# Performance work log

Measured on AMD Instinct MI355X. Metric: run time of the kernel, lower is better.

## Reference

```python
import jax, jax.numpy as jnp
import numpy as np

C, S, K, SIGMA = 512, 11, 3, 16
B = 128
EPS = 1e-5  # BatchNorm eps (eval mode, running_mean=0, running_var=1)


def _make_dct_weight(Cc, H, W):
    # FcaNet 'low16' frequency selection
    lx = [0, 0, 1, 1, 0, 2, 2, 1, 2, 0, 3, 4, 0, 1, 3, 0]
    ly = [0, 1, 0, 1, 2, 0, 1, 2, 2, 3, 0, 0, 4, 3, 1, 5]
    mx = [u * (H // 7) for u in lx]
    my = [v * (W // 7) for v in ly]
    w = np.zeros((Cc, H, W), np.float32)
    cp = Cc // len(lx)

    def bf(pos, freq, POS):
        r = np.cos(np.pi * freq * (pos + 0.5) / POS) / np.sqrt(POS)
        return r if freq == 0 else r * np.sqrt(2.0)

    for i, (u, v) in enumerate(zip(mx, my)):
        for tx in range(H):
            for ty in range(W):
                w[i * cp:(i + 1) * cp, tx, ty] = bf(tx, u, H) * bf(ty, v, W)
    return jnp.asarray(w)


def _bn(f, g, b):
    # eval-mode BatchNorm2d: (f - 0)/sqrt(1+eps)*g + b, per channel (axis 1)
    s = g / jnp.sqrt(1.0 + EPS)
    return f * s[None, :, None, None] + b[None, :, None, None]


def _conv1x1(f, w, b):
    return jnp.einsum('bchw,oc->bohw', f, w) + b[None, :, None, None]


def _spatial_kernel(f, w_conv, b_conv, g_sp, b_sp):
    Bn = f.shape[0]
    s = _conv1x1(f, w_conv, b_conv)                  # (B, K*K, S, S)
    s = s.reshape(Bn, K * K, S * S).transpose(0, 2, 1)  # (B, S*S, K*K)
    s = _bn(s.reshape(Bn, S * S, K, K), g_sp, b_sp)
    return s.reshape(Bn, S * S, K * K)


def _channel_kernel(f, dct_w, fc1, fc2, g_ch, b_ch):
    y = jnp.sum(f * dct_w[None], axis=(-2, -1))      # (B, C) DCT pooling
    y = jax.nn.sigmoid(jax.nn.relu(y @ fc1.T) @ fc2.T)  # (B, C*K*K)
    y = _bn(y.reshape(-1, C, K, K), g_ch, b_ch)
    return y.reshape(-1, C, K * K)


def _unfold(f):
    # torch-style per-pixel kxk neighborhoods -> (B, C, H, W, K, K)
    p = (K + 1) // 2 - 1
    Bn, Cn, H, W = f.shape
    fp = jnp.pad(f, ((0, 0), (0, 0), (p, p), (p, p)))
    pat = jnp.stack([fp[:, :, di:di + H, dj:dj + W]
                     for di in range(K) for dj in range(K)], axis=-1)
    return pat.reshape(Bn, Cn, H, W, K, K)


def setup_inputs() -> dict:
    key = jax.random.key(0)
    ks = iter(jax.random.split(key, 32))

    def nrm(shape, s=0.02):
        return s * jax.random.normal(next(ks), shape, jnp.float32)

    def gma(shape):
        return 1.0 + 0.1 * jax.random.normal(next(ks), shape, jnp.float32)

    return dict(
        x=jax.random.normal(next(ks), (B, C, S, S), jnp.float32),
        dct_w=_make_dct_weight(C, S, S),
        w_conv=nrm((K * K, C)), b_conv=nrm((K * K,)),
        g_sp=gma((S * S,)), b_sp=nrm((S * S,), 0.05),
        g_ch=gma((C,)), b_ch=nrm((C,), 0.05),
        fc1=nrm((C // SIGMA, C)), fc2=nrm((C * K * K, C // SIGMA)),
        up_w1=nrm((2 * C, C)), up_b1=nrm((2 * C,)), up_g1=gma((2 * C,)), up_bb1=nrm((2 * C,), 0.05),
        up_w2=nrm((2 * C, 2 * C)), up_b2=nrm((2 * C,)), up_g2=gma((2 * C,)), up_bb2=nrm((2 * C,), 0.05),
        lo_w1=nrm((2 * C, 2 * C)), lo_b1=nrm((2 * C,)), lo_g1=gma((2 * C,)), lo_bb1=nrm((2 * C,), 0.05),
        lo_w2=nrm((C, 2 * C)), lo_b2=nrm((C,)), lo_g2=gma((C,)), lo_bb2=nrm((C,), 0.05),
    )


def reference(x, dct_w, w_conv, b_conv, g_sp, b_sp, g_ch, b_ch, fc1, fc2,
              up_w1, up_b1, up_g1, up_bb1, up_w2, up_b2, up_g2, up_bb2,
              lo_w1, lo_b1, lo_g1, lo_bb1, lo_w2, lo_b2, lo_g2, lo_bb2):
    Bn = x.shape[0]
    # instance kernel: spatial (B,1,HW,KK) x channel (B,C,1,KK)
    sk = _spatial_kernel(x, w_conv, b_conv, g_sp, b_sp)[:, None]
    ck = _channel_kernel(x, dct_w, fc1, fc2, g_ch, b_ch)[:, :, None]
    inst = (sk * ck).reshape(Bn, C, S, S, K, K)
    # CLM task representation (sum over batch between upper and lower)
    a = jax.nn.relu(_bn(_conv1x1(x, up_w1, up_b1), up_g1, up_bb1))
    a = jax.nn.relu(_bn(_conv1x1(a, up_w2, up_b2), up_g2, up_bb2))
    a = a.sum(axis=0, keepdims=True)
    a = jax.nn.relu(_bn(_conv1x1(a, lo_w1, lo_b1), lo_g1, lo_bb1))
    task_s = jax.nn.sigmoid(_bn(_conv1x1(a, lo_w2, lo_b2), lo_g2, lo_bb2))
    # task kernel (shared across the batch)
    sk_t = _spatial_kernel(task_s, w_conv, b_conv, g_sp, b_sp)[:, None]
    ck_t = _channel_kernel(task_s, dct_w, fc1, fc2, g_ch, b_ch)[:, :, None]
    task_kernel = (sk_t * ck_t).reshape(1, C, S, S, K, K)
    kernel = task_kernel * inst
    adapted = (_unfold(x) * kernel).mean(axis=(-1, -2))  # (B,C,S,S)
    return adapted + x, task_kernel
```

## Files before the change

### kernel.cpp

```cpp
#include <hip/hip_runtime.h>
#include <hip/hip_bf16.h>
#include <math.h>

#define BNEPS 1e-5f
#define BDIM_B 128
#define CDIM 512
#define SS 121
#define KK 9
#define MROWS (BDIM_B * SS)

typedef unsigned short u16;
typedef __bf16 bf16x8 __attribute__((ext_vector_type(8)));
typedef float f32x4 __attribute__((ext_vector_type(4)));

__device__ __forceinline__ u16 f2bf(float f) {
    union { float f; unsigned int u; } v; v.f = f;
    unsigned int r = v.u + 0x7FFF + ((v.u >> 16) & 1);
    return (u16)(r >> 16);
}
__device__ __forceinline__ float bf2f(u16 v) {
    union { unsigned int u; float f; } x; x.u = ((unsigned int)v) << 16; return x.f;
}

__device__ __forceinline__ void gld16(const u16* g, u16* l) {
    __builtin_amdgcn_global_load_lds(
        (const __attribute__((address_space(1))) void*)g,
        (__attribute__((address_space(3))) void*)l, 16, 0, 0);
}

template<int MODE, int SWIZ>
__global__ __launch_bounds__(256)
void gemm_mfma(const u16* __restrict__ A, const u16* __restrict__ Bw,
               const float* __restrict__ bias, const float* __restrict__ g,
               const float* __restrict__ bb, void* __restrict__ out,
               int Kd, int N, int NT)
{
    __shared__ __align__(16) u16 Als[2][128 * 32];
    __shared__ __align__(16) u16 Bls[2][128 * 32];

    const int tid  = threadIdx.x;
    const int lane = tid & 63;
    const int w    = tid >> 6;
    const int wm   = w >> 1, wn = w & 1;

    int bx, by;
    if (SWIZ) {
        int i = blockIdx.x;
        if (i < 960) {
            int xg = i & 7;
            int j  = i >> 3;
            bx = xg * 15 + (j >> 3);
            by = j & 7;
        } else { bx = 120; by = i - 960; }
    } else {
        bx = blockIdx.x / NT; by = blockIdx.x - bx * NT;
    }
    const int bm = bx * 128;
    const int bn = by * 128;

    f32x4 acc[4][4] = {};

    const int subrow = tid >> 2;
    const int kq     = tid & 3;
    const int gchunk = kq ^ ((subrow >> 1) & 3);
    const u16* Ab = A  + (size_t)(bm + subrow) * Kd + gchunk * 8;
    const u16* Bb = Bw + (size_t)(bn + subrow) * Kd + gchunk * 8;

    const int fa_row = wm * 64 + (lane & 15);
    const int fb_row = wn * 64 + (lane & 15);
    const int kofs   = (((lane >> 4) ^ (((lane & 15) >> 1) & 3))) * 8;

    const int NK = Kd >> 5;

#define STG(bf_, t_) do { \
    gld16(Ab + (size_t)(t_) * 32,                 &Als[bf_][(w * 16) * 32]); \
    gld16(Ab + (size_t)64 * Kd + (size_t)(t_) * 32, &Als[bf_][(w * 16 + 64) * 32]); \
    gld16(Bb + (size_t)(t_) * 32,                 &Bls[bf_][(w * 16) * 32]); \
    gld16(Bb + (size_t)64 * Kd + (size_t)(t_) * 32, &Bls[bf_][(w * 16 + 64) * 32]); \
} while (0)

    STG(0, 0);
    __syncthreads();
    int cur = 0;
    for (int t = 0; t < NK; ++t) {
        if (t + 1 < NK) STG(cur ^ 1, t + 1);
        bf16x8 af[4], bfv[4];
        #pragma unroll
        for (int i = 0; i < 4; ++i)
            af[i] = *(const bf16x8*)&Als[cur][(fa_row + i * 16) * 32 + kofs];
        #pragma unroll
        for (int j = 0; j < 4; ++j)
            bfv[j] = *(const bf16x8*)&Bls[cur][(fb_row + j * 16) * 32 + kofs];
        #pragma unroll
        for (int i = 0; i < 4; ++i)
            #pragma unroll
            for (int j = 0; j < 4; ++j)
                acc[i][j] = __builtin_amdgcn_mfma_f32_16x16x32_bf16(af[i], bfv[j], acc[i][j], 0, 0, 0);
        __syncthreads();
        cur ^= 1;
    }
#undef STG

    const float inv = 1.0f / sqrtf(1.0f + BNEPS);

    if (MODE == 1) {
        u16* Y = (u16*)out;
        int dstrow[4][4];
        #pragma unroll
        for (int i = 0; i < 4; ++i) {
            int mb = bm + wm * 64 + i * 16 + (lane >> 4) * 4;
            #pragma unroll
            for (int r = 0; r < 4; ++r) {
                int m = mb + r;
                int b = m / 121, p = m - b * 121;
                dstrow[i][r] = p * 128 + b;
            }
        }
        #pragma unroll
        for (int j = 0; j < 4; ++j) {
            int n = bn + wn * 64 + j * 16 + (lane & 15);
            float sc = g[n] * inv, bo = bias[n], bv = bb[n];
            #pragma unroll
            for (int i = 0; i < 4; ++i)
                #pragma unroll
                for (int r = 0; r < 4; ++r) {
                    float v = (acc[i][j][r] + bo) * sc + bv;
                    v = fmaxf(v, 0.0f);
                    Y[(size_t)dstrow[i][r] * N + n] = f2bf(v);
                }
        }
    } else {
        float ps[4];
        #pragma unroll
        for (int j = 0; j < 4; ++j) {
            int n = bn + wn * 64 + j * 16 + (lane & 15);
            float sc = g[n] * inv, bo = bias[n], bv = bb[n];
            float s = 0.f;
            #pragma unroll
            for (int i = 0; i < 4; ++i)
                #pragma unroll
                for (int r = 0; r < 4; ++r) {
                    float v = (acc[i][j][r] + bo) * sc + bv;
                    s += fmaxf(v, 0.0f);
                }
            ps[j] = s;
        }
        __syncthreads();
        float* red = (float*)Als;
        #pragma unroll
        for (int j = 0; j < 4; ++j)
            red[(wm * 4 + (lane >> 4)) * 128 + wn * 64 + j * 16 + (lane & 15)] = ps[j];
        __syncthreads();
        if (tid < 128) {
            float s = 0.f;
            #pragma unroll
            for (int r = 0; r < 8; ++r) s += red[r * 128 + tid];
            ((u16*)out)[(size_t)bx * N + bn + tid] = f2bf(s);
        }
    }
}

template<int MODE>
__device__ __forceinline__ void gemm_small_body(
    const u16* __restrict__ A, const u16* __restrict__ Bw,
    const float* __restrict__ bias, const float* __restrict__ g,
    const float* __restrict__ bb, u16* __restrict__ Y,
    int Kd, int N, int bn)
{
    const int tid  = threadIdx.x;
    const int lane = tid & 63;
    const int w    = tid >> 6;
    const int fr   = lane & 15;
    const int kq   = lane >> 4;
    const int r0   = w * 32;

    f32x4 acc[2][4] = {};
    const u16* a0p = A + (size_t)(r0 + fr) * Kd + kq * 8;
    const u16* a1p = a0p + (size_t)16 * Kd;
    const u16* bp  = Bw + (size_t)(bn + fr) * Kd + kq * 8;

    #pragma unroll 4
    for (int k0 = 0; k0 < Kd; k0 += 32) {
        bf16x8 a0 = *(const bf16x8*)(a0p + k0);
        bf16x8 a1 = *(const bf16x8*)(a1p + k0);
        #pragma unroll
        for (int j = 0; j < 4; ++j) {
            bf16x8 bv = *(const bf16x8*)(bp + (size_t)j * 16 * Kd + k0);
            acc[0][j] = __builtin_amdgcn_mfma_f32_16x16x32_bf16(a0, bv, acc[0][j], 0, 0, 0);
            acc[1][j] = __builtin_amdgcn_mfma_f32_16x16x32_bf16(a1, bv, acc[1][j], 0, 0, 0);
        }
    }

    const float inv = 1.0f / sqrtf(1.0f + BNEPS);
    #pragma unroll
    for (int j = 0; j < 4; ++j) {
        int n = bn + j * 16 + (lane & 15);
        float sc = g[n] * inv, bo = bias[n], bv = bb[n];
        #pragma unroll
        for (int t = 0; t < 2; ++t)
            #pragma unroll
            for (int r = 0; r < 4; ++r) {
                int m = r0 + t * 16 + (lane >> 4) * 4 + r;
                float v = (acc[t][j][r] + bo) * sc + bv;
                if (MODE == 3) v = fmaxf(v, 0.0f);
                else           v = 1.f / (1.f + expf(-v));
                Y[(size_t)m * N + n] = f2bf(v);
            }
    }
}

template<int MODE>
__global__ __launch_bounds__(256)
void gemm_small(const u16* __restrict__ A, const u16* __restrict__ Bw,
                const float* __restrict__ bias, const float* __restrict__ g,
                const float* __restrict__ bb, u16* __restrict__ Y,
                int Kd, int N)
{
    gemm_small_body<MODE>(A, Bw, bias, g, bb, Y, Kd, N, blockIdx.x * 64);
}

__device__ __forceinline__ void spatial_body(
    const u16* __restrict__ Arow, const u16* __restrict__ wcb,
    const float* __restrict__ b_conv, const float* __restrict__ g_sp,
    const float* __restrict__ b_sp, float* __restrict__ skb,
    bool task, int blk, float* __restrict__ skt)
{
    const float inv = 1.0f / sqrtf(1.0f + BNEPS);
    const int tid  = threadIdx.x;
    const int lane = tid & 63;
    const int w    = tid >> 6;
    const int fr   = lane & 15;
    const int kq   = lane >> 4;
    const int r0   = w * 32;

    f32x4 acc0 = {}, acc1 = {};
    const u16* a0p = Arow + (size_t)(r0 + fr) * 512 + kq * 8;
    const u16* a1p = a0p + (size_t)16 * 512;
    const u16* bp  = wcb + (size_t)fr * 512 + kq * 8;
    #pragma unroll
    for (int k0 = 0; k0 < 512; k0 += 32) {
        bf16x8 a0 = *(const bf16x8*)(a0p + k0);
        bf16x8 a1 = *(const bf16x8*)(a1p + k0);
        bf16x8 b  = *(const bf16x8*)(bp + k0);
        acc0 = __builtin_amdgcn_mfma_f32_16x16x32_bf16(a0, b, acc0, 0, 0, 0);
        acc1 = __builtin_amdgcn_mfma_f32_16x16x32_bf16(a1, b, acc1, 0, 0, 0);
    }

    int n = lane & 15;
    if (n < 9) {
        float bo = b_conv[n];
        #pragma unroll
        for (int t = 0; t < 2; ++t) {
            f32x4 a = t ? acc1 : acc0;
            #pragma unroll
            for (int r = 0; r < 4; ++r) {
                int mloc = r0 + t * 16 + (lane >> 4) * 4 + r;
                if (!task) {
                    int m = blk * 128 + mloc;
                    int p = m % 121;
                    float v = (a[r] + bo) * (g_sp[p] * inv) + b_sp[p];
                    skb[(size_t)m * 9 + n] = v;
                } else if (mloc < 121) {
                    float v = (a[r] + bo) * (g_sp[mloc] * inv) + b_sp[mloc];
                    skt[(size_t)mloc * 9 + n] = v;
                }
            }
        }
    }
}

__device__ __forceinline__ void channel_body(
    const u16* __restrict__ src, const float* __restrict__ dctT,
    const float* __restrict__ fc1, const float* __restrict__ fc2,
    const float* __restrict__ g_ch, const float* __restrict__ b_ch,
    float* __restrict__ outp, float* yls, float* y2ls)
{
    const float inv = 1.0f / sqrtf(1.0f + BNEPS);

    {
        int c = threadIdx.x * 2;
        float s0 = 0.f, s1 = 0.f;
        for (int p = 0; p < SS; ++p) {
            unsigned v = *(const unsigned*)(src + (size_t)p * 512 + c);
            float2 d  = *(const float2*)(dctT + (size_t)p * 512 + c);
            s0 += bf2f((u16)(v & 0xFFFFu)) * d.x;
            s1 += bf2f((u16)(v >> 16)) * d.y;
        }
        yls[c] = s0; yls[c + 1] = s1;
    }
    __syncthreads();

    {
        int o = threadIdx.x >> 3, kp = threadIdx.x & 7;
        const float* w = fc1 + (size_t)o * 512;
        float s = 0.f;
        for (int k = kp * 4; k < 512; k += 32) {
            float4 wv = *(const float4*)(w + k);
            float4 av = *(const float4*)(yls + k);
            s += wv.x * av.x + wv.y * av.y + wv.z * av.z + wv.w * av.w;
        }
        s += __shfl_xor(s, 1);
        s += __shfl_xor(s, 2);
        s += __shfl_xor(s, 4);
        if (kp == 0) y2ls[o] = fmaxf(s, 0.f);
    }
    __syncthreads();

    for (int o = threadIdx.x; o < CDIM * KK; o += 256) {
        const float* w = fc2 + (size_t)o * 32;
        float s = 0.f;
        #pragma unroll
        for (int k = 0; k < 32; ++k) s += y2ls[k] * w[k];
        s = 1.f / (1.f + expf(-s));
        int c = o / KK;
        s = s * (g_ch[c] * inv) + b_ch[c];
        outp[o] = s;
    }
}

__global__ __launch_bounds__(256)
void lo1_spatial(const u16* __restrict__ asum_b, const u16* __restrict__ lw1b,
                 const float* __restrict__ lo_b1, const float* __restrict__ lo_g1,
                 const float* __restrict__ lo_bb1, u16* __restrict__ a3b,
                 const u16* __restrict__ Xb, const u16* __restrict__ wcb,
                 const float* __restrict__ b_conv, const float* __restrict__ g_sp,
                 const float* __restrict__ b_sp, const float* __restrict__ dctT,
                 const float* __restrict__ fc1, const float* __restrict__ fc2,
                 const float* __restrict__ g_ch, const float* __restrict__ b_ch,
                 float* __restrict__ skb, float* __restrict__ ckbuf)
{
    __shared__ float sm[544];
    int bi = blockIdx.x;
    if (bi < 16) {
        gemm_small_body<3>(asum_b, lw1b, lo_b1, lo_g1, lo_bb1, a3b, 1024, 1024, bi * 64);
        return;
    }
    bi -= 16;
    if (bi < 121) {
        spatial_body(Xb + (size_t)bi * 128 * 512, wcb, b_conv, g_sp, b_sp, skb, false, bi, nullptr);
        return;
    }
    bi -= 121;
    channel_body(Xb + (size_t)bi * 121 * 512, dctT, fc1, fc2, g_ch, b_ch,
                 ckbuf + (size_t)bi * CDIM * KK, sm, sm + 512);
}

__global__ __launch_bounds__(256)
void task_combo(const u16* __restrict__ ts_pc, const u16* __restrict__ wcb,
                const float* __restrict__ b_conv, const float* __restrict__ g_sp,
                const float* __restrict__ b_sp, const float* __restrict__ dctT,
                const float* __restrict__ fc1, const float* __restrict__ fc2,
                const float* __restrict__ g_ch, const float* __restrict__ b_ch,
                float* __restrict__ skt, float* __restrict__ ck_t)
{
    __shared__ float sm[544];
    if (blockIdx.x == 0)
        spatial_body(ts_pc, wcb, b_conv, g_sp, b_sp, nullptr, true, 0, skt);
    else
        channel_body(ts_pc, dctT, fc1, fc2, g_ch, b_ch, ck_t, sm, sm + 512);
}

#define W1N (1024 * 512)
#define W2N (1024 * 1024)
#define L1N (1024 * 1024)
#define L2N (512 * 1024)
#define VECN ((W1N + W2N + L1N + L2N) / 4)
#define DCTN (512 * 121)
#define WCN (16 * 512)
#define PREP_ELEM (VECN + DCTN + WCN)
#define PREP_BLKS (1024 + (PREP_ELEM + 255) / 256)
__global__ void prep_combo(const float* __restrict__ x, u16* __restrict__ Xb,
                           const float* __restrict__ w1, const float* __restrict__ w2,
                           const float* __restrict__ l1, const float* __restrict__ l2,
                           const float* __restrict__ dct, const float* __restrict__ w_conv,
                           u16* __restrict__ o1, u16* __restrict__ o2,
                           u16* __restrict__ o3, u16* __restrict__ o4,
                           float* __restrict__ dctT, u16* __restrict__ wcb)
{
    __shared__ float t[64 * 121];
    if (blockIdx.x < 1024) {
        int b = blockIdx.x >> 3, c0 = (blockIdx.x & 7) * 64;
        for (int idx = threadIdx.x; idx < 64 * 121; idx += 256) {
            int c = idx / 121, p = idx - c * 121;
            t[idx] = x[((size_t)b * 512 + c0 + c) * 121 + p];
        }
        __syncthreads();
        for (int idx = threadIdx.x; idx < 121 * 64; idx += 256) {
            int p = idx >> 6, c = idx & 63;
            Xb[((size_t)(b * 121 + p)) * 512 + c0 + c] = f2bf(t[c * 121 + p]);
        }
        return;
    }
    int i = (blockIdx.x - 1024) * 256 + threadIdx.x;
    if (i < VECN) {
        int q = i;
        const float* s; u16* d;
        if (q < W1N / 4)                    { s = w1; d = o1; }
        else if (q < (W1N + W2N) / 4)       { s = w2; d = o2; q -= W1N / 4; }
        else if (q < (W1N + W2N + L1N) / 4) { s = l1; d = o3; q -= (W1N + W2N) / 4; }
        else                                { s = l2; d = o4; q -= (W1N + W2N + L1N) / 4; }
        float4 v = ((const float4*)s)[q];
        uint2 r;
        r.x = (unsigned)f2bf(v.x) | ((unsigned)f2bf(v.y) << 16);
        r.y = (unsigned)f2bf(v.z) | ((unsigned)f2bf(v.w) << 16);
        ((uint2*)d)[q] = r;
        return;
    }
    i -= VECN;
    if (i < DCTN) {
        int p = i >> 9, c = i & 511;
        dctT[i] = dct[(size_t)c * 121 + p];
        return;
    }
    i -= DCTN;
    if (i < WCN) {
        int n = i >> 9, c = i & 511;
        wcb[i] = (n < 9) ? f2bf(w_conv[(size_t)n * 512 + c]) : (u16)0;
    }
}

#define TKN (CDIM * SS * KK)
#define FIN_BLKS (1024 + (TKN + 255) / 256)
__global__ __launch_bounds__(256)
void final_combo(const float* __restrict__ x, const float* __restrict__ skb,
                 const float* __restrict__ sk_t, const float* __restrict__ ckbuf,
                 const float* __restrict__ ck_t, float* __restrict__ out0,
                 float* __restrict__ tk)
{
    __shared__ float PS[SS * KK];
    __shared__ float CS[64 * KK];
    __shared__ float XT[64 * SS];

    if (blockIdx.x >= 1024) {
        int idx = (blockIdx.x - 1024) * 256 + threadIdx.x;
        if (idx < TKN) {
            int k9 = idx % KK;
            int pc = idx / KK;
            int p = pc % SS, c = pc / SS;
            tk[idx] = sk_t[p * KK + k9] * ck_t[c * KK + k9];
        }
        return;
    }

    const int tid = threadIdx.x;
    const int b = blockIdx.x >> 3, c0 = (blockIdx.x & 7) * 64;

    const float* sp = skb + (size_t)b * SS * KK;
    for (int i = tid; i < SS * KK; i += 256) PS[i] = sp[i] * sk_t[i];
    const float* cp = ckbuf + ((size_t)b * CDIM + c0) * KK;
    const float* tp = ck_t + (size_t)c0 * KK;
    for (int i = tid; i < (64 * KK) / 4; i += 256) {
        float4 a = ((const float4*)cp)[i];
        float4 bq = ((const float4*)tp)[i];
        float4 r; r.x = a.x * bq.x; r.y = a.y * bq.y; r.z = a.z * bq.z; r.w = a.w * bq.w;
        ((float4*)CS)[i] = r;
    }
    const float* xp = x + ((size_t)b * CDIM + c0) * SS;
    for (int i = tid; i < (64 * SS) / 4; i += 256)
        ((float4*)XT)[i] = ((const float4*)xp)[i];
    __syncthreads();

    float* op = out0 + ((size_t)b * CDIM + c0) * SS;
    for (int ci = tid; ci < (64 * SS) / 4; ci += 256) {
        float4 o;
        #pragma unroll
        for (int r = 0; r < 4; ++r) {
            int i = ci * 4 + r;
            int c = i / SS, p = i - c * SS;
            int h = p / 11, w = p - h * 11;
            const float* xc = XT + c * SS;
            const float* ps = PS + p * KK;
            const float* cs = CS + c * KK;
            float acc = 0.f;
            #pragma unroll
            for (int di = 0; di < 3; ++di) {
                int hh = h + di - 1;
                bool hv = (unsigned)hh < 11u;
                #pragma unroll
                for (int dj = 0; dj < 3; ++dj) {
                    int ww = w + dj - 1;
                    int k = di * 3 + dj;
                    float xv = (hv && (unsigned)ww < 11u) ? xc[hh * 11 + ww] : 0.f;
                    acc += xv * ps[k] * cs[k];
                }
            }
            ((float*)&o)[r] = acc * (1.0f / 9.0f) + xc[p];
        }
        ((float4*)op)[ci] = o;
    }
}

extern "C" void kernel_launch(void* const* d_in, const int* in_sizes, int n_in,
                              void* d_out, int out_size, void* d_ws, size_t ws_size,
                              hipStream_t stream)
{
    const float* x      = (const float*)d_in[0];
    const float* dct_w  = (const float*)d_in[1];
    const float* w_conv = (const float*)d_in[2];
    const float* b_conv = (const float*)d_in[3];
    const float* g_sp   = (const float*)d_in[4];
    const float* b_sp   = (const float*)d_in[5];
    const float* g_ch   = (const float*)d_in[6];
    const float* b_ch   = (const float*)d_in[7];
    const float* fc1    = (const float*)d_in[8];
    const float* fc2    = (const float*)d_in[9];
    const float* up_w1  = (const float*)d_in[10];
    const float* up_b1  = (const float*)d_in[11];
    const float* up_g1  = (const float*)d_in[12];
    const float* up_bb1 = (const float*)d_in[13];
    const float* up_w2  = (const float*)d_in[14];
    const float* up_b2  = (const float*)d_in[15];
    const float* up_g2  = (const float*)d_in[16];
    const float* up_bb2 = (const float*)d_in[17];
    const float* lo_w1  = (const float*)d_in[18];
    const float* lo_b1  = (const float*)d_in[19];
    const float* lo_g1  = (const float*)d_in[20];
    const float* lo_bb1 = (const float*)d_in[21];
    const float* lo_w2  = (const float*)d_in[22];
    const float* lo_b2  = (const float*)d_in[23];
    const float* lo_g2  = (const float*)d_in[24];
    const float* lo_bb2 = (const float*)d_in[25];

    float* out0 = (float*)d_out;
    float* tk   = out0 + (size_t)BDIM_B * CDIM * SS;

    char* ws = (char*)d_ws;
    size_t off = 0;
    auto alloc = [&](size_t bytes) { void* p = ws + off; off += (bytes + 63) & ~(size_t)63; return p; };
    u16*   Xb      = (u16*)alloc((size_t)MROWS * 512 * 2);
    u16*   Y1      = (u16*)alloc((size_t)MROWS * 1024 * 2);
    u16*   w1b     = (u16*)alloc((size_t)W1N * 2);
    u16*   w2b     = (u16*)alloc((size_t)W2N * 2);
    u16*   lw1b    = (u16*)alloc((size_t)L1N * 2);
    u16*   lw2b    = (u16*)alloc((size_t)L2N * 2);
    u16*   asum_b  = (u16*)alloc((size_t)128 * 1024 * 2);
    u16*   a3b     = (u16*)alloc((size_t)128 * 1024 * 2);
    u16*   ts_pc   = (u16*)alloc((size_t)128 * 512 * 2);
    float* dctT    = (float*)alloc((size_t)SS * 512 * 4);
    u16*   wcb     = (u16*)alloc((size_t)WCN * 2);
    float* ckbuf   = (float*)alloc((size_t)BDIM_B * CDIM * KK * 4);
    float* skbuf   = (float*)alloc((size_t)BDIM_B * SS * KK * 4);
    float* ck_t    = (float*)alloc((size_t)CDIM * KK * 4);
    float* sk_t    = (float*)alloc((size_t)SS * KK * 4);

    hipLaunchKernelGGL(prep_combo, dim3(PREP_BLKS), dim3(256), 0, stream,
                       x, Xb, up_w1, up_w2, lo_w1, lo_w2, dct_w, w_conv,
                       w1b, w2b, lw1b, lw2b, dctT, wcb);

    hipLaunchKernelGGL((gemm_mfma<1, 1>), dim3(121 * 8), dim3(256), 0, stream,
                       Xb, w1b, up_b1, up_g1, up_bb1, (void*)Y1, 512, 1024, 8);
    hipLaunchKernelGGL((gemm_mfma<2, 1>), dim3(121 * 8), dim3(256), 0, stream,
                       Y1, w2b, up_b2, up_g2, up_bb2, (void*)asum_b, 1024, 1024, 8);

    hipLaunchKernelGGL(lo1_spatial, dim3(16 + 121 + 128), dim3(256), 0, stream,
                       asum_b, lw1b, lo_b1, lo_g1, lo_bb1, a3b,
                       Xb, wcb, b_conv, g_sp, b_sp,
                       dctT, fc1, fc2, g_ch, b_ch,
                       skbuf, ckbuf);

    hipLaunchKernelGGL((gemm_small<4>), dim3(8), dim3(256), 0, stream,
                       a3b, lw2b, lo_b2, lo_g2, lo_bb2, ts_pc, 1024, 512);

    hipLaunchKernelGGL(task_combo, dim3(2), dim3(256), 0, stream,
                       ts_pc, wcb, b_conv, g_sp, b_sp,
                       dctT, fc1, fc2, g_ch, b_ch, sk_t, ck_t);

    hipLaunchKernelGGL(final_combo, dim3(FIN_BLKS), dim3(256), 0, stream,
                       x, skbuf, sk_t, ckbuf, ck_t, out0, tk);
}
```

Measured before the change: 349.7 us.

## Drop GEMM double-buffer prefetch for 64-wide K steps; regroup small kernels

```diff
diff --git a/kernel.cpp b/kernel.cpp
--- a/kernel.cpp
+++ b/kernel.cpp
@@ -65,41 +65,49 @@
     const int gchunk = kq ^ ((subrow >> 1) & 3);
     const u16* Ab = A  + (size_t)(bm + subrow) * Kd + gchunk * 8;
     const u16* Bb = Bw + (size_t)(bn + subrow) * Kd + gchunk * 8;
+    u16* Al0  = &Als[0][(w * 16) * 32];
+    u16* Al1  = &Als[0][(w * 16 + 64) * 32];
+    u16* Bl0  = &Bls[0][(w * 16) * 32];
+    u16* Bl1  = &Bls[0][(w * 16 + 64) * 32];
+    u16* Al0b = &Als[1][(w * 16) * 32];
+    u16* Al1b = &Als[1][(w * 16 + 64) * 32];
+    u16* Bl0b = &Bls[1][(w * 16) * 32];
+    u16* Bl1b = &Bls[1][(w * 16 + 64) * 32];
 
     const int fa_row = wm * 64 + (lane & 15);
     const int fb_row = wn * 64 + (lane & 15);
     const int kofs   = (((lane >> 4) ^ (((lane & 15) >> 1) & 3))) * 8;
 
-    const int NK = Kd >> 5;
-
-#define STG(bf_, t_) do { \
-    gld16(Ab + (size_t)(t_) * 32,                 &Als[bf_][(w * 16) * 32]); \
-    gld16(Ab + (size_t)64 * Kd + (size_t)(t_) * 32, &Als[bf_][(w * 16 + 64) * 32]); \
-    gld16(Bb + (size_t)(t_) * 32,                 &Bls[bf_][(w * 16) * 32]); \
-    gld16(Bb + (size_t)64 * Kd + (size_t)(t_) * 32, &Bls[bf_][(w * 16 + 64) * 32]); \
-} while (0)
-
-    STG(0, 0);
-    __syncthreads();
-    int cur = 0;
-    for (int t = 0; t < NK; ++t) {
-        if (t + 1 < NK) STG(cur ^ 1, t + 1);
-        bf16x8 af[4], bfv[4];
-        #pragma unroll
-        for (int i = 0; i < 4; ++i)
-            af[i] = *(const bf16x8*)&Als[cur][(fa_row + i * 16) * 32 + kofs];
-        #pragma unroll
-        for (int j = 0; j < 4; ++j)
-            bfv[j] = *(const bf16x8*)&Bls[cur][(fb_row + j * 16) * 32 + kofs];
-        #pragma unroll
-        for (int i = 0; i < 4; ++i)
+    for (int k0 = 0; k0 < Kd; k0 += 64) {
+        __syncthreads();
+        gld16(Ab + k0,                      Al0);
+        gld16(Ab + (size_t)64 * Kd + k0,    Al1);
+        gld16(Bb + k0,                      Bl0);
+        gld16(Bb + (size_t)64 * Kd + k0,    Bl1);
+        gld16(Ab + k0 + 32,                 Al0b);
+        gld16(Ab + (size_t)64 * Kd + k0 + 32, Al1b);
+        gld16(Bb + k0 + 32,                 Bl0b);
+        gld16(Bb + (size_t)64 * Kd + k0 + 32, Bl1b);
+        __syncthreads();
+
+        #pragma unroll
+        for (int hb = 0; hb < 2; ++hb) {
+            const u16* Ah = &Als[hb][0];
+            const u16* Bh = &Bls[hb][0];
+            bf16x8 af[4], bfv[4];
+            #pragma unroll
+            for (int i = 0; i < 4; ++i)
+                af[i] = *(const bf16x8*)&Ah[(fa_row + i * 16) * 32 + kofs];
             #pragma unroll
             for (int j = 0; j < 4; ++j)
-                acc[i][j] = __builtin_amdgcn_mfma_f32_16x16x32_bf16(af[i], bfv[j], acc[i][j], 0, 0, 0);
-        __syncthreads();
-        cur ^= 1;
-    }
-#undef STG
+                bfv[j] = *(const bf16x8*)&Bh[(fb_row + j * 16) * 32 + kofs];
+            #pragma unroll
+            for (int i = 0; i < 4; ++i)
+                #pragma unroll
+                for (int j = 0; j < 4; ++j)
+                    acc[i][j] = __builtin_amdgcn_mfma_f32_16x16x32_bf16(af[i], bfv[j], acc[i][j], 0, 0, 0);
+        }
+    }
 
     const float inv = 1.0f / sqrtf(1.0f + BNEPS);
 
@@ -161,12 +169,13 @@
 }
 
 template<int MODE>
-__device__ __forceinline__ void gemm_small_body(
-    const u16* __restrict__ A, const u16* __restrict__ Bw,
-    const float* __restrict__ bias, const float* __restrict__ g,
-    const float* __restrict__ bb, u16* __restrict__ Y,
-    int Kd, int N, int bn)
-{
+__global__ __launch_bounds__(256)
+void gemm_small(const u16* __restrict__ A, const u16* __restrict__ Bw,
+                const float* __restrict__ bias, const float* __restrict__ g,
+                const float* __restrict__ bb, u16* __restrict__ Y,
+                int Kd, int N)
+{
+    const int bn   = blockIdx.x * 64;
     const int tid  = threadIdx.x;
     const int lane = tid & 63;
     const int w    = tid >> 6;
@@ -207,16 +216,6 @@
                 Y[(size_t)m * N + n] = f2bf(v);
             }
     }
-}
-
-template<int MODE>
-__global__ __launch_bounds__(256)
-void gemm_small(const u16* __restrict__ A, const u16* __restrict__ Bw,
-                const float* __restrict__ bias, const float* __restrict__ g,
-                const float* __restrict__ bb, u16* __restrict__ Y,
-                int Kd, int N)
-{
-    gemm_small_body<MODE>(A, Bw, bias, g, bb, Y, Kd, N, blockIdx.x * 64);
 }
 
 __device__ __forceinline__ void spatial_body(
@@ -319,45 +318,26 @@
 }
 
 __global__ __launch_bounds__(256)
-void lo1_spatial(const u16* __restrict__ asum_b, const u16* __restrict__ lw1b,
-                 const float* __restrict__ lo_b1, const float* __restrict__ lo_g1,
-                 const float* __restrict__ lo_bb1, u16* __restrict__ a3b,
-                 const u16* __restrict__ Xb, const u16* __restrict__ wcb,
-                 const float* __restrict__ b_conv, const float* __restrict__ g_sp,
-                 const float* __restrict__ b_sp, const float* __restrict__ dctT,
-                 const float* __restrict__ fc1, const float* __restrict__ fc2,
-                 const float* __restrict__ g_ch, const float* __restrict__ b_ch,
-                 float* __restrict__ skb, float* __restrict__ ckbuf)
+void spatial_ck_combo(const u16* __restrict__ Xb, const u16* __restrict__ Xt,
+                      const u16* __restrict__ wcb, const float* __restrict__ b_conv,
+                      const float* __restrict__ g_sp, const float* __restrict__ b_sp,
+                      const float* __restrict__ dctT,
+                      const float* __restrict__ fc1, const float* __restrict__ fc2,
+                      const float* __restrict__ g_ch, const float* __restrict__ b_ch,
+                      float* __restrict__ skb, float* __restrict__ skt,
+                      float* __restrict__ ckbuf, float* __restrict__ ck_t)
 {
     __shared__ float sm[544];
-    int bi = blockIdx.x;
-    if (bi < 16) {
-        gemm_small_body<3>(asum_b, lw1b, lo_b1, lo_g1, lo_bb1, a3b, 1024, 1024, bi * 64);
+    if (blockIdx.x < 122) {
+        const bool task = (blockIdx.x == 121);
+        spatial_body(task ? Xt : Xb + (size_t)blockIdx.x * 128 * 512,
+                     wcb, b_conv, g_sp, b_sp, skb, task, blockIdx.x, skt);
         return;
     }
-    bi -= 16;
-    if (bi < 121) {
-        spatial_body(Xb + (size_t)bi * 128 * 512, wcb, b_conv, g_sp, b_sp, skb, false, bi, nullptr);
-        return;
-    }
-    bi -= 121;
-    channel_body(Xb + (size_t)bi * 121 * 512, dctT, fc1, fc2, g_ch, b_ch,
-                 ckbuf + (size_t)bi * CDIM * KK, sm, sm + 512);
-}
-
-__global__ __launch_bounds__(256)
-void task_combo(const u16* __restrict__ ts_pc, const u16* __restrict__ wcb,
-                const float* __restrict__ b_conv, const float* __restrict__ g_sp,
-                const float* __restrict__ b_sp, const float* __restrict__ dctT,
-                const float* __restrict__ fc1, const float* __restrict__ fc2,
-                const float* __restrict__ g_ch, const float* __restrict__ b_ch,
-                float* __restrict__ skt, float* __restrict__ ck_t)
-{
-    __shared__ float sm[544];
-    if (blockIdx.x == 0)
-        spatial_body(ts_pc, wcb, b_conv, g_sp, b_sp, nullptr, true, 0, skt);
-    else
-        channel_body(ts_pc, dctT, fc1, fc2, g_ch, b_ch, ck_t, sm, sm + 512);
+    const int g = blockIdx.x - 122;
+    const u16* src = (g < 128) ? Xb + (size_t)g * 121 * 512 : Xt;
+    channel_body(src, dctT, fc1, fc2, g_ch, b_ch,
+                 (g < 128) ? ckbuf + (size_t)g * CDIM * KK : ck_t, sm, sm + 512);
 }
 
 #define W1N (1024 * 512)
@@ -552,18 +532,15 @@
     hipLaunchKernelGGL((gemm_mfma<2, 1>), dim3(121 * 8), dim3(256), 0, stream,
                        Y1, w2b, up_b2, up_g2, up_bb2, (void*)asum_b, 1024, 1024, 8);
 
-    hipLaunchKernelGGL(lo1_spatial, dim3(16 + 121 + 128), dim3(256), 0, stream,
-                       asum_b, lw1b, lo_b1, lo_g1, lo_bb1, a3b,
-                       Xb, wcb, b_conv, g_sp, b_sp,
-                       dctT, fc1, fc2, g_ch, b_ch,
-                       skbuf, ckbuf);
-
+    hipLaunchKernelGGL((gemm_small<3>), dim3(16), dim3(256), 0, stream,
+                       asum_b, lw1b, lo_b1, lo_g1, lo_bb1, a3b, 1024, 1024);
     hipLaunchKernelGGL((gemm_small<4>), dim3(8), dim3(256), 0, stream,
                        a3b, lw2b, lo_b2, lo_g2, lo_bb2, ts_pc, 1024, 512);
 
-    hipLaunchKernelGGL(task_combo, dim3(2), dim3(256), 0, stream,
-                       ts_pc, wcb, b_conv, g_sp, b_sp,
-                       dctT, fc1, fc2, g_ch, b_ch, sk_t, ck_t);
+    hipLaunchKernelGGL(spatial_ck_combo, dim3(122 + 129), dim3(256), 0, stream,
+                       Xb, ts_pc, wcb, b_conv, g_sp, b_sp,
+                       dctT, fc1, fc2, g_ch, b_ch,
+                       skbuf, sk_t, ckbuf, ck_t);
 
     hipLaunchKernelGGL(final_combo, dim3(FIN_BLKS), dim3(256), 0, stream,
                        x, skbuf, sk_t, ckbuf, ck_t, out0, tk);
```

After: 327.1 us. 1.07x faster.
